# Kernel optimization log

Hardware: AMD Instinct MI355X
Metric: run time of the kernel (lower is better)

## Reference

```python
import jax, jax.numpy as jnp
import numpy as np
from jax import lax

VOCAB = 28996  # bert-base-cased vocab size (static for segment_sum)
B, S, D = 32, 512, 768
NUM_CLASSES = 9


def _lstm_dir(x, w_ih, w_hh, b_ih, b_hh):
    # x: [T, N, In]; torch gate order i, f, g, o packed along dim 0 of weights
    T, N, _ = x.shape
    H = w_hh.shape[1]
    xg = jnp.einsum('tni,gi->tng', x, w_ih) + b_ih  # precompute input projections [T,N,4H]

    def step(carry, xg_t):
        h, c = carry
        g = xg_t + h @ w_hh.T + b_hh
        i, f, gg, o = jnp.split(g, 4, axis=-1)
        c = jax.nn.sigmoid(f) * c + jax.nn.sigmoid(i) * jnp.tanh(gg)
        h = jax.nn.sigmoid(o) * jnp.tanh(c)
        return (h, c), h

    h0 = jnp.zeros((N, H), x.dtype)
    _, ys = lax.scan(step, (h0, h0), xg)
    return ys  # [T, N, H]


def setup_inputs() -> dict:
    key = jax.random.key(0)
    ks = jax.random.split(key, 8)
    H, In = D, 2 * D
    w = 0.02
    return {
        'batch': jax.random.randint(ks[0], (B, S), 0, VOCAB),
        'hidden': jax.random.normal(ks[1], (B, S, D), jnp.float32),
        'w_ih_f': jax.random.normal(ks[2], (4 * H, In), jnp.float32) * w,
        'w_hh_f': jax.random.normal(ks[3], (4 * H, H), jnp.float32) * w,
        'b_ih_f': jnp.zeros((4 * H,), jnp.float32),
        'b_hh_f': jnp.zeros((4 * H,), jnp.float32),
        'w_ih_b': jax.random.normal(ks[4], (4 * H, In), jnp.float32) * w,
        'w_hh_b': jax.random.normal(ks[5], (4 * H, H), jnp.float32) * w,
        'b_ih_b': jnp.zeros((4 * H,), jnp.float32),
        'b_hh_b': jnp.zeros((4 * H,), jnp.float32),
        'lin_w': jax.random.normal(ks[6], (NUM_CLASSES, 2 * H), jnp.float32) * w,
        'lin_b': jnp.zeros((NUM_CLASSES,), jnp.float32),
    }


def reference(batch, hidden, w_ih_f, w_hh_f, b_ih_f, b_hh_f,
              w_ih_b, w_hh_b, b_ih_b, b_hh_b, lin_w, lin_b):
    b, s, d = hidden.shape
    flat_ids = batch.reshape(-1)            # [B*S]
    flat_h = hidden.reshape(-1, d)          # [B*S, D]
    # segment mean of embeddings grouped by raw token id (the dict loop in torch)
    sums = jax.ops.segment_sum(flat_h, flat_ids, num_segments=VOCAB)
    counts = jax.ops.segment_sum(jnp.ones((flat_ids.shape[0], 1), hidden.dtype),
                                 flat_ids, num_segments=VOCAB)
    means = sums / jnp.maximum(counts, 1.0)
    ctx = means[flat_ids].reshape(b, s, d)  # gather-broadcast back per position
    x = jnp.concatenate([hidden, ctx], axis=2)  # [B, S, 2D]
    # nn.LSTM is not batch_first: scans over dim0 (B acts as time, S as batch)
    out_f = _lstm_dir(x, w_ih_f, w_hh_f, b_ih_f, b_hh_f)
    out_b = _lstm_dir(x[::-1], w_ih_b, w_hh_b, b_ih_b, b_hh_b)[::-1]
    out = jnp.concatenate([out_f, out_b], axis=-1)  # [B, S, 2D]
    # dropout is identity in eval mode
    return out @ lin_w.T + lin_b  # [B, S, num_classes]
```

## Files before the change

### kernel.cpp

```cpp
#include <hip/hip_runtime.h>

#define VOCAB 28996
#define BB 32
#define SS 512
#define DD 768
#define NCLS 9
#define ROWS (BB*SS)
#define IN2 (2*DD)
#define G4 (4*DD)
#define NB2 (2*G4)

typedef __attribute__((ext_vector_type(8))) short short8;
typedef __attribute__((ext_vector_type(4))) short shortx4;
typedef __attribute__((ext_vector_type(4))) float floatx4;
typedef unsigned long long ull;

__device__ __forceinline__ float bf2f(unsigned short u){
  union { unsigned int i; float f; } v; v.i = ((unsigned int)u) << 16; return v.f;
}
__device__ __forceinline__ unsigned short f2bf(float f){
  union { float f; unsigned int i; } v; v.f = f;
  unsigned int r = v.i + 0x7FFFu + ((v.i >> 16) & 1u);
  return (unsigned short)(r >> 16);
}
__device__ __forceinline__ float sigf(float x){ return 1.0f / (1.0f + __expf(-x)); }
__device__ __forceinline__ float tanhfast(float x){
  float y = fminf(fmaxf(x, -15.f), 15.f);
  float e = __expf(2.f * y);
  return 1.f - 2.f / (e + 1.f);
}

__device__ __forceinline__ void gl_lds16(const unsigned short* g, unsigned short* l){
  __builtin_amdgcn_global_load_lds((__attribute__((address_space(1))) void*)(g),
                                   (__attribute__((address_space(3))) void*)(l), 16, 0, 0);
}
__device__ __forceinline__ void gl_lds16_c(const unsigned short* g, unsigned short* l){
  __builtin_amdgcn_global_load_lds((__attribute__((address_space(1))) void*)(g),
                                   (__attribute__((address_space(3))) void*)(l), 16, 0, 17);
}
__device__ __forceinline__ void store16_sc1(unsigned short* p, short8 v){
  asm volatile("global_store_dwordx4 %0, %1, off sc0 sc1" :: "v"(p), "v"(v) : "memory");
}

__device__ __forceinline__ void grid_bar(unsigned* bar, int nb)
{
  __syncthreads();
  if (threadIdx.x == 0) {
    unsigned g = __hip_atomic_load(bar + 1, __ATOMIC_RELAXED, __HIP_MEMORY_SCOPE_AGENT);
    unsigned a = __hip_atomic_fetch_add(bar, 1u, __ATOMIC_RELAXED, __HIP_MEMORY_SCOPE_AGENT);
    if (a == (unsigned)(nb - 1)) {
      __hip_atomic_store(bar, 0u, __ATOMIC_RELAXED, __HIP_MEMORY_SCOPE_AGENT);
      __hip_atomic_store(bar + 1, g + 1u, __ATOMIC_RELEASE, __HIP_MEMORY_SCOPE_AGENT);
    } else {
      unsigned cur;
      do {
        __builtin_amdgcn_s_sleep(2);
        cur = __hip_atomic_load(bar + 1, __ATOMIC_RELAXED, __HIP_MEMORY_SCOPE_AGENT);
      } while (cur == g);
    }
  }
  __syncthreads();
}

__global__ void seg_scatter(const int* __restrict__ ids, const float* __restrict__ hidden,
                            float* __restrict__ sums, float* __restrict__ counts)
{
  int r = blockIdx.x;
  int id = ids[r];
  const float* h = hidden + (long)r * DD;
  float* s = sums + (long)id * DD;
  for (int d = threadIdx.x; d < DD; d += 256)
    atomicAdd(&s[d], h[d]);
  if (threadIdx.x == 0) atomicAdd(&counts[id], 1.0f);
}

__global__ void build_x(const int* __restrict__ ids, const float* __restrict__ hidden,
                        const float* __restrict__ sums, const float* __restrict__ counts,
                        unsigned short* __restrict__ x)
{
  int r = blockIdx.x;
  int id = ids[r];
  float inv = 1.0f / fmaxf(counts[id], 1.0f);
  const float* h = hidden + (long)r * DD;
  const float* s = sums + (long)id * DD;
  unsigned short* xr = x + (long)r * IN2;
  for (int d = threadIdx.x; d < DD; d += 256) {
    xr[d]      = f2bf(h[d]);
    xr[DD + d] = f2bf(s[d] * inv);
  }
}

__global__ void conv_w_perm(const float* __restrict__ w, unsigned short* __restrict__ o, int K)
{
  long i = (long)blockIdx.x * 256 + threadIdx.x;
  if (i >= (long)G4 * K) return;
  int row = (int)(i / K); int k = (int)(i - (long)row * K);
  int u = row >> 2, g = row & 3;
  o[i] = f2bf(w[((long)(g * DD + u)) * K + k]);
}

__global__ void conv_bias_perm(const float* __restrict__ bif, const float* __restrict__ bhf,
                               const float* __restrict__ bib, const float* __restrict__ bhb,
                               float* __restrict__ o)
{
  int n = blockIdx.x * 256 + threadIdx.x;
  if (n >= NB2) return;
  int d = n / G4, rr = n - d * G4, u = rr >> 2, g = rr & 3;
  int s = g * DD + u;
  o[n] = d ? (bib[s] + bhb[s]) : (bif[s] + bhf[s]);
}

__global__ __launch_bounds__(256, 2)
void gemm_bt(const unsigned short* __restrict__ A, int lda,
             const unsigned short* __restrict__ B, int ldb,
             unsigned short* __restrict__ C, int ldc,
             const float* __restrict__ bias, int K)
{
  __shared__ unsigned short lA[128 * 32];
  __shared__ unsigned short lB[128 * 32];
  const int t = threadIdx.x;
  const int lane = t & 63;
  const int wv = t >> 6;
  const int wm = wv >> 1, wn = wv & 1;
  const int l15 = lane & 15, q = lane >> 4;
  const long m0 = (long)blockIdx.y * 128;
  const long n0 = (long)blockIdx.x * 128;
  const int rowS = t >> 2;
  const int kc = (((t & 3) ^ ((t >> 3) & 3))) * 8;
  const int qsw = (q ^ ((l15 >> 1) & 3)) * 8;
  const unsigned short* gA = A + (m0 + rowS) * lda + kc;
  const unsigned short* gB = B + (n0 + rowS) * ldb + kc;
  unsigned short* dA0 = lA + (wv << 9);
  unsigned short* dA1 = lA + 2048 + (wv << 9);
  unsigned short* dB0 = lB + (wv << 9);
  unsigned short* dB1 = lB + 2048 + (wv << 9);

  floatx4 acc[4][4];
  #pragma unroll
  for (int i = 0; i < 4; i++)
    #pragma unroll
    for (int j = 0; j < 4; j++)
      acc[i][j] = (floatx4){0.f, 0.f, 0.f, 0.f};

  const long a64 = (long)64 * lda;
  const long b64 = (long)64 * ldb;
  for (int kt = 0; kt < K; kt += 32) {
    gl_lds16(gA + kt,       dA0);
    gl_lds16(gA + a64 + kt, dA1);
    gl_lds16(gB + kt,       dB0);
    gl_lds16(gB + b64 + kt, dB1);
    __syncthreads();
    short8 af[4], bfr[4];
    #pragma unroll
    for (int i = 0; i < 4; i++)
      af[i] = *(const short8*)(lA + (wm * 64 + i * 16 + l15) * 32 + qsw);
    #pragma unroll
    for (int j = 0; j < 4; j++)
      bfr[j] = *(const short8*)(lB + (wn * 64 + j * 16 + l15) * 32 + qsw);
    #pragma unroll
    for (int i = 0; i < 4; i++)
      #pragma unroll
      for (int j = 0; j < 4; j++)
        acc[i][j] = __builtin_amdgcn_mfma_f32_16x16x32_bf16(af[i], bfr[j], acc[i][j], 0, 0, 0);
    __syncthreads();
  }

  #pragma unroll
  for (int i = 0; i < 4; i++) {
    #pragma unroll
    for (int j = 0; j < 4; j++) {
      const long mg = m0 + wm * 64 + i * 16 + q * 4;
      const long ng = n0 + wn * 64 + j * 16 + l15;
      const float bb = bias[ng];
      #pragma unroll
      for (int r = 0; r < 4; r++)
        C[(mg + r) * ldc + ng] = f2bf(acc[i][j][r] + bb);
    }
  }
}

__global__ __launch_bounds__(256, 1)
void lstm_persist(const unsigned short* __restrict__ xg, int ldxg,
                  const unsigned short* __restrict__ whh,
                  unsigned short* __restrict__ hbuf,
                  unsigned short* __restrict__ outc,
                  unsigned* bar,
                  int dir0, int ndir)
{
  __shared__ unsigned short bufA[16384];
  __shared__ unsigned short bufB[16384];
  __shared__ unsigned short xgs[16384];
  __shared__ unsigned short hout[128 * 40];

  const int bid = blockIdx.x;
  const int xcd = bid & 7;
  const int idx = bid >> 3;
  int dm, k3;
  if (ndir == 2) { dm = idx & 7; k3 = idx >> 3; }
  else           { dm = idx & 3; k3 = idx >> 2; }
  const int ld  = (ndir == 2) ? (dm & 1) : 0;
  const int dir = dir0 + ld;
  const int mt  = (ndir == 2) ? (dm >> 1) : dm;
  const int nt  = k3 * 8 + xcd;
  const int m0 = mt * 128, n0 = nt * 128;
  const int u0 = n0 >> 2;
  unsigned* gbar = bar + dm * 16;

  const int t0 = threadIdx.x;
  const int lane = t0 & 63;
  const int wv = t0 >> 6;
  const int wm = wv >> 1, wn = wv & 1;
  const int l15 = lane & 15, q = lane >> 4;
  const long ldoff = (ndir == 2 && ld == 1) ? (long)G4 : 0;

  const unsigned short* Bdir = whh + (long)dir * G4 * DD;
  const int scolA = (((lane & 3) ^ ((lane >> 3) & 3))) * 8;
  const int qsw   = (q ^ ((l15 >> 1) & 3)) * 8;
  const int xsw   = l15 << 3;
  const int xsrc  = (((t0 & 15) ^ ((t0 >> 4) & 15))) * 8;

  float c_reg[4][4];
  #pragma unroll
  for (int i = 0; i < 4; i++)
    #pragma unroll
    for (int j = 0; j < 4; j++)
      c_reg[i][j] = 0.f;

  for (int s = 0; s < BB; s++) {
    const int tt = dir ? (BB - 1 - s) : s;
    const unsigned short* hRead = hbuf + (((long)(s & 1)) * ndir + ld) * ((long)SS * DD);
    unsigned short* hw = hbuf + (((long)((s + 1) & 1)) * ndir + ld) * ((long)SS * DD);

    {
      const unsigned short* xrow = xg + ((long)tt * SS + m0) * ldxg + ldoff + n0;
      #pragma unroll
      for (int c = 0; c < 8; c++) {
        int row = c * 16 + (t0 >> 4);
        gl_lds16(xrow + (long)row * ldxg + xsrc,
                 xgs + c * 2048 + wv * 512 + lane * 8);
      }
    }

    floatx4 acc[4][4];
    #pragma unroll
    for (int i = 0; i < 4; i++)
      #pragma unroll
      for (int j = 0; j < 4; j++)
        acc[i][j] = (floatx4){0.f, 0.f, 0.f, 0.f};

    for (int kt = 0; kt < 6; kt++) {
      const int kb = kt << 7;
      #pragma unroll
      for (int p = 0; p < 4; p++)
        #pragma unroll
        for (int rbh = 0; rbh < 2; rbh++) {
          int rb = (wv * 2 + rbh) * 16 + (lane >> 2);
          gl_lds16_c(hRead + (long)(m0 + rb) * DD + kb + p * 32 + scolA,
                     bufA + p * 4096 + (wv * 2 + rbh) * 512 + lane * 8);
          gl_lds16(Bdir + (long)(n0 + rb) * DD + kb + p * 32 + scolA,
                   bufB + p * 4096 + (wv * 2 + rbh) * 512 + lane * 8);
        }
      __syncthreads();
      #pragma unroll
      for (int ks = 0; ks < 4; ks++) {
        short8 af[4], bfr[4];
        #pragma unroll
        for (int i = 0; i < 4; i++)
          af[i] = *(const short8*)(bufA + ks * 4096 + (wm * 64 + i * 16 + l15) * 32 + qsw);
        #pragma unroll
        for (int j = 0; j < 4; j++)
          bfr[j] = *(const short8*)(bufB + ks * 4096 + (wn * 64 + j * 16 + l15) * 32 + qsw);
        #pragma unroll
        for (int i = 0; i < 4; i++)
          #pragma unroll
          for (int j = 0; j < 4; j++)
            acc[i][j] = __builtin_amdgcn_mfma_f32_16x16x32_bf16(bfr[j], af[i], acc[i][j], 0, 0, 0);
      }
      __syncthreads();
    }

    #pragma unroll
    for (int i = 0; i < 4; i++) {
      const int mrow = wm * 64 + i * 16 + l15;
      const int xbase = mrow * 128;
      #pragma unroll
      for (int j = 0; j < 4; j++) {
        const int nb = wn * 64 + j * 16 + q * 4;
        shortx4 xv = *(const shortx4*)(xgs + xbase + (nb ^ xsw));
        float gi = acc[i][j][0] + bf2f((unsigned short)xv[0]);
        float gf = acc[i][j][1] + bf2f((unsigned short)xv[1]);
        float gg = acc[i][j][2] + bf2f((unsigned short)xv[2]);
        float go = acc[i][j][3] + bf2f((unsigned short)xv[3]);
        float c = sigf(gf) * c_reg[i][j] + sigf(gi) * tanhfast(gg);
        float h = sigf(go) * tanhfast(c);
        c_reg[i][j] = c;
        hout[mrow * 40 + (nb >> 2)] = f2bf(h);
      }
    }
    __syncthreads();
    {
      const int row = t0 >> 1;
      const int half = t0 & 1;
      const unsigned short* src = hout + row * 40 + half * 16;
      short8 v0 = *(const short8*)(src);
      short8 v1 = *(const short8*)(src + 8);
      unsigned short* hwp = hw + (long)(m0 + row) * DD + u0 + half * 16;
      unsigned short* op  = outc + ((long)tt * SS + m0 + row) * IN2 + dir * DD + u0 + half * 16;
      store16_sc1(hwp, v0);
      store16_sc1(hwp + 8, v1);
      *(short8*)op = v0;
      *(short8*)(op + 8) = v1;
    }
    asm volatile("s_waitcnt vmcnt(0)" ::: "memory");
    if (s < BB - 1) grid_bar(gbar, 24);
  }
}

__global__ void final_linear(const unsigned short* __restrict__ xin, const float* __restrict__ w,
                             const float* __restrict__ b, float* __restrict__ out)
{
  __shared__ float red[NCLS * 256];
  int row = blockIdx.x;
  const unsigned short* x = xin + (long)row * IN2;
  float p[NCLS];
  #pragma unroll
  for (int c = 0; c < NCLS; c++) p[c] = 0.f;
  for (int k = threadIdx.x; k < IN2; k += 256) {
    float xv = bf2f(x[k]);
    #pragma unroll
    for (int c = 0; c < NCLS; c++) p[c] += xv * w[c * IN2 + k];
  }
  #pragma unroll
  for (int c = 0; c < NCLS; c++) red[c * 256 + threadIdx.x] = p[c];
  __syncthreads();
  for (int s = 128; s > 0; s >>= 1) {
    if (threadIdx.x < s) {
      #pragma unroll
      for (int c = 0; c < NCLS; c++)
        red[c * 256 + threadIdx.x] += red[c * 256 + threadIdx.x + s];
    }
    __syncthreads();
  }
  if (threadIdx.x < NCLS)
    out[(long)row * NCLS + threadIdx.x] = red[threadIdx.x * 256] + b[threadIdx.x];
}

extern "C" void kernel_launch(void* const* d_in, const int* in_sizes, int n_in,
                              void* d_out, int out_size, void* d_ws, size_t ws_size,
                              hipStream_t stream)
{
  const int*   batch  = (const int*)d_in[0];
  const float* hidden = (const float*)d_in[1];
  const float* w_ih_f = (const float*)d_in[2];
  const float* w_hh_f = (const float*)d_in[3];
  const float* b_ih_f = (const float*)d_in[4];
  const float* b_hh_f = (const float*)d_in[5];
  const float* w_ih_b = (const float*)d_in[6];
  const float* w_hh_b = (const float*)d_in[7];
  const float* b_ih_b = (const float*)d_in[8];
  const float* b_hh_b = (const float*)d_in[9];
  const float* lin_w  = (const float*)d_in[10];
  const float* lin_b  = (const float*)d_in[11];
  float* out = (float*)d_out;

  char* ws = (char*)d_ws;
  size_t off = 0;
  auto alloc = [&](size_t bytes) -> char* {
    char* p = ws + off;
    off += (bytes + 255) & ~(size_t)255;
    return p;
  };

  const size_t SZ_XG_A = (size_t)ROWS * NB2 * 2;
  const size_t SZ_XG_B = (size_t)ROWS * G4  * 2;
  const size_t SZ_XBF  = (size_t)ROWS * IN2 * 2;
  const size_t SZ_W    = (size_t)G4 * IN2 * 2;
  const size_t SZ_BIAS = (size_t)NB2 * 4;
  const size_t SZ_HBUF = (size_t)2 * 2 * SS * DD * 2;
  const size_t SZ_BAR  = 512;
  const size_t SZ_SUMS = (size_t)VOCAB * DD * 4 + (size_t)VOCAB * 4;

  const size_t NEED_C = SZ_XG_A + SZ_XBF + SZ_W + SZ_BIAS + SZ_HBUF + SZ_BAR + 8 * 256;
  const bool combined = ws_size >= NEED_C;

  const long nWIH = (long)G4 * IN2;
  const long nWHH = (long)G4 * DD;

  if (combined) {
    unsigned short* xg   = (unsigned short*)alloc(SZ_XG_A);
    unsigned short* xbf  = (unsigned short*)alloc(SZ_XBF);
    unsigned short* wbuf = (unsigned short*)alloc(SZ_W);
    float*          bias = (float*)alloc(SZ_BIAS);
    unsigned short* hbuf = (unsigned short*)alloc(SZ_HBUF);
    unsigned*       bar  = (unsigned*)alloc(SZ_BAR);
    float* sums   = (float*)xg;
    float* counts = sums + (size_t)VOCAB * DD;

    hipMemsetAsync(sums, 0, SZ_SUMS, stream);
    hipMemsetAsync(bar, 0, SZ_BAR, stream);
    seg_scatter<<<ROWS, 256, 0, stream>>>(batch, hidden, sums, counts);
    build_x<<<ROWS, 256, 0, stream>>>(batch, hidden, sums, counts, xbf);
    conv_bias_perm<<<(NB2 + 255) / 256, 256, 0, stream>>>(b_ih_f, b_hh_f, b_ih_b, b_hh_b, bias);

    for (int dir = 0; dir < 2; dir++) {
      conv_w_perm<<<(unsigned)((nWIH + 255) / 256), 256, 0, stream>>>(dir ? w_ih_b : w_ih_f, wbuf, IN2);
      dim3 grid(G4 / 128, ROWS / 128, 1);
      gemm_bt<<<grid, 256, 0, stream>>>(xbf, IN2, wbuf, IN2,
                                        xg + (size_t)dir * G4, NB2,
                                        bias + (size_t)dir * G4, IN2);
    }
    conv_w_perm<<<(unsigned)((nWHH + 255) / 256), 256, 0, stream>>>(w_hh_f, wbuf, DD);
    conv_w_perm<<<(unsigned)((nWHH + 255) / 256), 256, 0, stream>>>(w_hh_b, wbuf + (size_t)G4 * DD, DD);

    hipMemsetAsync(hbuf, 0, SZ_HBUF, stream);
    lstm_persist<<<192, 256, 0, stream>>>(xg, NB2, wbuf, hbuf, xbf, bar, 0, 2);
    final_linear<<<ROWS, 256, 0, stream>>>(xbf, lin_w, lin_b, out);
  } else {
    unsigned short* xg   = (unsigned short*)alloc(SZ_XG_B);
    unsigned short* xbf  = (unsigned short*)alloc(SZ_XBF);
    unsigned short* outc = (unsigned short*)alloc(SZ_XBF);
    unsigned short* wih  = (unsigned short*)alloc(SZ_W);
    unsigned short* whh  = (unsigned short*)alloc(SZ_W);
    float*          bias = (float*)alloc(SZ_BIAS);
    unsigned short* hbuf = (unsigned short*)alloc(SZ_HBUF);
    unsigned*       bar  = (unsigned*)alloc(SZ_BAR);
    float* sums   = (float*)xg;
    float* counts = sums + (size_t)VOCAB * DD;

    hipMemsetAsync(sums, 0, SZ_SUMS, stream);
    hipMemsetAsync(bar, 0, SZ_BAR, stream);
    seg_scatter<<<ROWS, 256, 0, stream>>>(batch, hidden, sums, counts);
    build_x<<<ROWS, 256, 0, stream>>>(batch, hidden, sums, counts, xbf);
    conv_bias_perm<<<(NB2 + 255) / 256, 256, 0, stream>>>(b_ih_f, b_hh_f, b_ih_b, b_hh_b, bias);
    conv_w_perm<<<(unsigned)((nWHH + 255) / 256), 256, 0, stream>>>(w_hh_f, whh, DD);
    conv_w_perm<<<(unsigned)((nWHH + 255) / 256), 256, 0, stream>>>(w_hh_b, whh + (size_t)G4 * DD, DD);

    for (int dir = 0; dir < 2; dir++) {
      conv_w_perm<<<(unsigned)((nWIH + 255) / 256), 256, 0, stream>>>(dir ? w_ih_b : w_ih_f, wih, IN2);
      {
        dim3 grid(G4 / 128, ROWS / 128, 1);
        gemm_bt<<<grid, 256, 0, stream>>>(xbf, IN2, wih, IN2, xg, G4,
                                          bias + (size_t)dir * G4, IN2);
      }
      hipMemsetAsync(hbuf, 0, SZ_HBUF, stream);
      lstm_persist<<<96, 256, 0, stream>>>(xg, G4, whh, hbuf, outc, bar, dir, 1);
    }
    final_linear<<<ROWS, 256, 0, stream>>>(outc, lin_w, lin_b, out);
  }
}
```

Before: 1.310 ms.

## Double the LSTM block to 512 threads and prefetch next step's gate inputs

The persistent LSTM kernel now runs 8 waves per block instead of 4, so each wave covers a 32x64 output sub-tile and holds half the accumulators and cell state. The input-projection tile for the next timestep is double-buffered in LDS and loaded before the grid barrier, taking that load off the critical path of the following step. The extra waves are meant to hide the latency of the per-step matmul and its loads, at the cost of 32KB more LDS and more threads taking part in each block barrier.

```diff
diff --git a/kernel.cpp b/kernel.cpp
--- a/kernel.cpp
+++ b/kernel.cpp
@@ -179,7 +179,7 @@
   }
 }
 
-__global__ __launch_bounds__(256, 1)
+__global__ __launch_bounds__(512, 1)
 void lstm_persist(const unsigned short* __restrict__ xg, int ldxg,
                   const unsigned short* __restrict__ whh,
                   unsigned short* __restrict__ hbuf,
@@ -189,7 +189,7 @@
 {
   __shared__ unsigned short bufA[16384];
   __shared__ unsigned short bufB[16384];
-  __shared__ unsigned short xgs[16384];
+  __shared__ unsigned short xgs[2][16384];
   __shared__ unsigned short hout[128 * 40];
 
   const int bid = blockIdx.x;
@@ -209,69 +209,71 @@
   const int t0 = threadIdx.x;
   const int lane = t0 & 63;
   const int wv = t0 >> 6;
-  const int wm = wv >> 1, wn = wv & 1;
+  const int wm = wv >> 1;
+  const int wn = wv & 1;
   const int l15 = lane & 15, q = lane >> 4;
   const long ldoff = (ndir == 2 && ld == 1) ? (long)G4 : 0;
 
   const unsigned short* Bdir = whh + (long)dir * G4 * DD;
+  const int srow  = lane >> 2;
   const int scolA = (((lane & 3) ^ ((lane >> 3) & 3))) * 8;
   const int qsw   = (q ^ ((l15 >> 1) & 3)) * 8;
   const int xsw   = l15 << 3;
   const int xsrc  = (((t0 & 15) ^ ((t0 >> 4) & 15))) * 8;
 
-  float c_reg[4][4];
+  float c_reg[2][4];
   #pragma unroll
-  for (int i = 0; i < 4; i++)
+  for (int i = 0; i < 2; i++)
     #pragma unroll
     for (int j = 0; j < 4; j++)
       c_reg[i][j] = 0.f;
+
+  {
+    const int tt0 = dir ? (BB - 1) : 0;
+    const unsigned short* xrow = xg + ((long)tt0 * SS + m0) * ldxg + ldoff + n0;
+    #pragma unroll
+    for (int c = 0; c < 4; c++) {
+      int row = c * 32 + (t0 >> 4);
+      gl_lds16(xrow + (long)row * ldxg + xsrc,
+               xgs[0] + c * 4096 + (t0 >> 4) * 128 + (t0 & 15) * 8);
+    }
+  }
 
   for (int s = 0; s < BB; s++) {
     const int tt = dir ? (BB - 1 - s) : s;
     const unsigned short* hRead = hbuf + (((long)(s & 1)) * ndir + ld) * ((long)SS * DD);
     unsigned short* hw = hbuf + (((long)((s + 1) & 1)) * ndir + ld) * ((long)SS * DD);
-
-    {
-      const unsigned short* xrow = xg + ((long)tt * SS + m0) * ldxg + ldoff + n0;
-      #pragma unroll
-      for (int c = 0; c < 8; c++) {
-        int row = c * 16 + (t0 >> 4);
-        gl_lds16(xrow + (long)row * ldxg + xsrc,
-                 xgs + c * 2048 + wv * 512 + lane * 8);
-      }
-    }
-
-    floatx4 acc[4][4];
-    #pragma unroll
-    for (int i = 0; i < 4; i++)
+    const unsigned short* xcur = xgs[s & 1];
+
+    floatx4 acc[2][4];
+    #pragma unroll
+    for (int i = 0; i < 2; i++)
       #pragma unroll
       for (int j = 0; j < 4; j++)
         acc[i][j] = (floatx4){0.f, 0.f, 0.f, 0.f};
 
     for (int kt = 0; kt < 6; kt++) {
       const int kb = kt << 7;
-      #pragma unroll
-      for (int p = 0; p < 4; p++)
+      const int rb = wv * 16 + srow;
+      #pragma unroll
+      for (int p = 0; p < 4; p++) {
+        gl_lds16_c(hRead + (long)(m0 + rb) * DD + kb + p * 32 + scolA,
+                   bufA + p * 4096 + wv * 512 + lane * 8);
+        gl_lds16(Bdir + (long)(n0 + rb) * DD + kb + p * 32 + scolA,
+                 bufB + p * 4096 + wv * 512 + lane * 8);
+      }
+      __syncthreads();
+      #pragma unroll
+      for (int ks = 0; ks < 4; ks++) {
+        short8 af[2], bfr[4];
         #pragma unroll
-        for (int rbh = 0; rbh < 2; rbh++) {
-          int rb = (wv * 2 + rbh) * 16 + (lane >> 2);
-          gl_lds16_c(hRead + (long)(m0 + rb) * DD + kb + p * 32 + scolA,
-                     bufA + p * 4096 + (wv * 2 + rbh) * 512 + lane * 8);
-          gl_lds16(Bdir + (long)(n0 + rb) * DD + kb + p * 32 + scolA,
-                   bufB + p * 4096 + (wv * 2 + rbh) * 512 + lane * 8);
-        }
-      __syncthreads();
-      #pragma unroll
-      for (int ks = 0; ks < 4; ks++) {
-        short8 af[4], bfr[4];
-        #pragma unroll
-        for (int i = 0; i < 4; i++)
-          af[i] = *(const short8*)(bufA + ks * 4096 + (wm * 64 + i * 16 + l15) * 32 + qsw);
+        for (int i = 0; i < 2; i++)
+          af[i] = *(const short8*)(bufA + ks * 4096 + (wm * 32 + i * 16 + l15) * 32 + qsw);
         #pragma unroll
         for (int j = 0; j < 4; j++)
           bfr[j] = *(const short8*)(bufB + ks * 4096 + (wn * 64 + j * 16 + l15) * 32 + qsw);
         #pragma unroll
-        for (int i = 0; i < 4; i++)
+        for (int i = 0; i < 2; i++)
           #pragma unroll
           for (int j = 0; j < 4; j++)
             acc[i][j] = __builtin_amdgcn_mfma_f32_16x16x32_bf16(bfr[j], af[i], acc[i][j], 0, 0, 0);
@@ -280,13 +282,13 @@
     }
 
     #pragma unroll
-    for (int i = 0; i < 4; i++) {
-      const int mrow = wm * 64 + i * 16 + l15;
+    for (int i = 0; i < 2; i++) {
+      const int mrow = wm * 32 + i * 16 + l15;
       const int xbase = mrow * 128;
       #pragma unroll
       for (int j = 0; j < 4; j++) {
         const int nb = wn * 64 + j * 16 + q * 4;
-        shortx4 xv = *(const shortx4*)(xgs + xbase + (nb ^ xsw));
+        shortx4 xv = *(const shortx4*)(xcur + xbase + (nb ^ xsw));
         float gi = acc[i][j][0] + bf2f((unsigned short)xv[0]);
         float gf = acc[i][j][1] + bf2f((unsigned short)xv[1]);
         float gg = acc[i][j][2] + bf2f((unsigned short)xv[2]);
@@ -299,20 +301,27 @@
     }
     __syncthreads();
     {
-      const int row = t0 >> 1;
-      const int half = t0 & 1;
-      const unsigned short* src = hout + row * 40 + half * 16;
-      short8 v0 = *(const short8*)(src);
-      short8 v1 = *(const short8*)(src + 8);
-      unsigned short* hwp = hw + (long)(m0 + row) * DD + u0 + half * 16;
-      unsigned short* op  = outc + ((long)tt * SS + m0 + row) * IN2 + dir * DD + u0 + half * 16;
+      const int row = t0 >> 2;
+      const int qq = t0 & 3;
+      short8 v0 = *(const short8*)(hout + row * 40 + qq * 8);
+      unsigned short* hwp = hw + (long)(m0 + row) * DD + u0 + qq * 8;
+      unsigned short* op  = outc + ((long)tt * SS + m0 + row) * IN2 + dir * DD + u0 + qq * 8;
       store16_sc1(hwp, v0);
-      store16_sc1(hwp + 8, v1);
       *(short8*)op = v0;
-      *(short8*)(op + 8) = v1;
     }
     asm volatile("s_waitcnt vmcnt(0)" ::: "memory");
-    if (s < BB - 1) grid_bar(gbar, 24);
+    if (s < BB - 1) {
+      const int tn = dir ? (BB - 2 - s) : (s + 1);
+      const unsigned short* xrow = xg + ((long)tn * SS + m0) * ldxg + ldoff + n0;
+      unsigned short* xnxt = xgs[(s + 1) & 1];
+      #pragma unroll
+      for (int c = 0; c < 4; c++) {
+        int row = c * 32 + (t0 >> 4);
+        gl_lds16(xrow + (long)row * ldxg + xsrc,
+                 xnxt + c * 4096 + (t0 >> 4) * 128 + (t0 & 15) * 8);
+      }
+      grid_bar(gbar, 24);
+    }
   }
 }
 
@@ -413,7 +422,7 @@
     conv_w_perm<<<(unsigned)((nWHH + 255) / 256), 256, 0, stream>>>(w_hh_b, wbuf + (size_t)G4 * DD, DD);
 
     hipMemsetAsync(hbuf, 0, SZ_HBUF, stream);
-    lstm_persist<<<192, 256, 0, stream>>>(xg, NB2, wbuf, hbuf, xbf, bar, 0, 2);
+    lstm_persist<<<192, 512, 0, stream>>>(xg, NB2, wbuf, hbuf, xbf, bar, 0, 2);
     final_linear<<<ROWS, 256, 0, stream>>>(xbf, lin_w, lin_b, out);
   } else {
     unsigned short* xg   = (unsigned short*)alloc(SZ_XG_B);
@@ -443,7 +452,7 @@
                                           bias + (size_t)dir * G4, IN2);
       }
       hipMemsetAsync(hbuf, 0, SZ_HBUF, stream);
-      lstm_persist<<<96, 256, 0, stream>>>(xg, G4, whh, hbuf, outc, bar, dir, 1);
+      lstm_persist<<<96, 512, 0, stream>>>(xg, G4, whh, hbuf, outc, bar, dir, 1);
     }
     final_linear<<<ROWS, 256, 0, stream>>>(outc, lin_w, lin_b, out);
   }
```

Result: faster. 1.251 ms (-4.5%).
